# Optimization experiments

Hardware: AMD Instinct MI355X
Metric: run time of the kernel (lower is better)

Reference implementation:

```python
import jax, jax.numpy as jnp
import numpy as np

N_NODES = 50000

def _gcn_layer(x, src, dst, W, b, n_nodes):
    # Linear transform first (PyG GCNConv): h = x @ W
    h = x @ W  # [N, out]
    # Add self-loops
    loop = jnp.arange(n_nodes, dtype=src.dtype)
    src2 = jnp.concatenate([src, loop])
    dst2 = jnp.concatenate([dst, loop])
    # Symmetric normalization deg^-1/2 (deg counts incoming edges incl. self-loop)
    deg = jax.ops.segment_sum(jnp.ones_like(dst2, dtype=h.dtype), dst2, num_segments=n_nodes)
    dinv = jnp.where(deg > 0, jax.lax.rsqrt(deg), 0.0)
    norm = dinv[src2] * dinv[dst2]  # [E+N]
    # Gather-scale-scatter aggregation
    msg = h[src2] * norm[:, None]  # [E+N, out]
    out = jax.ops.segment_sum(msg, dst2, num_segments=n_nodes)
    return out + b

def setup_inputs() -> dict:
    key = jax.random.key(0)
    k1, k2, k3, k4 = jax.random.split(key, 4)
    E = 800000
    x = jax.random.normal(k1, (N_NODES, 128), dtype=jnp.float32)
    edge_index = jax.random.randint(k2, (2, E), 0, N_NODES, dtype=jnp.int64)
    W1 = jax.random.normal(k3, (128, 512), dtype=jnp.float32) * (1.0 / np.sqrt(128))
    b1 = jnp.zeros((512,), dtype=jnp.float32)
    W2 = jax.random.normal(k4, (512, 250), dtype=jnp.float32) * (1.0 / np.sqrt(512))
    b2 = jnp.zeros((250,), dtype=jnp.float32)
    return {"x": x, "edge_index": edge_index, "W1": W1, "b1": b1, "W2": W2, "b2": b2}

def reference(x, edge_index, W1, b1, W2, b2):
    src, dst = edge_index[0], edge_index[1]
    h = _gcn_layer(x, src, dst, W1, b1, N_NODES)
    h = jax.nn.relu(h)
    h = _gcn_layer(h, src, dst, W2, b2, N_NODES)
    return jax.nn.relu(h)
```

## Files before the change

### kernel.cpp

```cpp
#include <hip/hip_runtime.h>

#define N_NODES 50000

typedef __attribute__((ext_vector_type(8))) short bf16x8;
typedef __attribute__((ext_vector_type(4))) float f32x4;

__device__ __forceinline__ ushort f2bf(float f) {
    union { float f; unsigned u; } v; v.f = f;
    unsigned r = v.u + 0x7fff + ((v.u >> 16) & 1);
    return (ushort)(r >> 16);
}
__device__ __forceinline__ float bf2f(ushort u) {
    union { unsigned u; float f; } v; v.u = ((unsigned)u) << 16;
    return v.f;
}
__device__ __forceinline__ float bf2f_lo(unsigned u) {
    union { unsigned u; float f; } v; v.u = u << 16;
    return v.f;
}
__device__ __forceinline__ float bf2f_hi(unsigned u) {
    union { unsigned u; float f; } v; v.u = u & 0xffff0000u;
    return v.f;
}

__global__ void k_detect(const void* ei, int* flag) {
    __shared__ int bad;
    if (threadIdx.x == 0) bad = 0;
    __syncthreads();
    long long v = ((const long long*)ei)[threadIdx.x];
    if (v < 0 || v >= N_NODES) atomicOr(&bad, 1);
    __syncthreads();
    if (threadIdx.x == 0) *flag = bad ? 0 : 1;
}

__device__ __forceinline__ int eload(const void* ei, int idx, int is64) {
    return is64 ? (int)((const long long*)ei)[idx] : ((const int*)ei)[idx];
}

__global__ void k_hist(const void* ei, const int* flag, int* deg, int e) {
    int i = blockIdx.x * blockDim.x + threadIdx.x;
    if (i >= e) return;
    int is64 = *flag;
    int d = eload(ei, e + i, is64);
    atomicAdd(&deg[d], 1);
}

__global__ __launch_bounds__(512)
void k_scanA(const int* __restrict__ deg, int* __restrict__ rp1,
             int* __restrict__ bsum, int n) {
    __shared__ int wsum[8];
    const int i = blockIdx.x * 512 + threadIdx.x;
    const int lane = threadIdx.x & 63, wid = threadIdx.x >> 6;
    int x = (i < n) ? deg[i] : 0;
    #pragma unroll
    for (int off = 1; off < 64; off <<= 1) {
        int y = __shfl_up(x, off, 64);
        if (lane >= off) x += y;
    }
    if (lane == 63) wsum[wid] = x;
    __syncthreads();
    if (wid == 0 && lane < 8) {
        int s = wsum[lane];
        #pragma unroll
        for (int off = 1; off < 8; off <<= 1) {
            int y = __shfl_up(s, off, 64);
            if (lane >= off) s += y;
        }
        wsum[lane] = s;
    }
    __syncthreads();
    int incl = x + (wid > 0 ? wsum[wid - 1] : 0);
    if (i < n) rp1[i] = incl;
    if (threadIdx.x == 0) bsum[blockIdx.x] = wsum[7];
}

__global__ void k_scanB(int* bsum, int nb) {
    __shared__ int ws2[2];
    const int lane = threadIdx.x & 63, wid = threadIdx.x >> 6;
    int x = (threadIdx.x < nb) ? bsum[threadIdx.x] : 0;
    #pragma unroll
    for (int off = 1; off < 64; off <<= 1) {
        int y = __shfl_up(x, off, 64);
        if (lane >= off) x += y;
    }
    if (lane == 63) ws2[wid] = x;
    __syncthreads();
    int incl = x + (wid > 0 ? ws2[0] : 0);
    if (threadIdx.x < nb) bsum[threadIdx.x] = incl;
}

__global__ __launch_bounds__(512)
void k_scanC(const int* __restrict__ deg, int* __restrict__ rowptr,
             const int* __restrict__ bsum, int* __restrict__ cur,
             float* __restrict__ dinv, int n) {
    const int i = blockIdx.x * 512 + threadIdx.x;
    if (i >= n) return;
    const int off = (blockIdx.x > 0) ? bsum[blockIdx.x - 1] : 0;
    const int d = deg[i];
    const int incl = rowptr[i + 1] + off;
    rowptr[i + 1] = incl;
    cur[i] = incl - d;
    dinv[i] = rsqrtf((float)(d + 1));
    if (i == 0) rowptr[0] = 0;
}

__global__ void k_fill(const void* ei, const int* flag, int* cur, int* adj, int e) {
    int i = blockIdx.x * blockDim.x + threadIdx.x;
    if (i >= e) return;
    int is64 = *flag;
    int s = eload(ei, i, is64);
    int d = eload(ei, e + i, is64);
    int pos = atomicAdd(&cur[d], 1);
    adj[pos] = s;
}

__global__ void k_splitT(const float* __restrict__ W, ushort* __restrict__ ohi,
                         ushort* __restrict__ olo, int R , int C ,
                         int Nout ) {
    int idx = blockIdx.x * blockDim.x + threadIdx.x;
    if (idx >= Nout * R) return;
    int n = idx / R;
    int k = idx - n * R;
    float v = (n < C) ? W[(size_t)k * C + n] : 0.0f;
    ushort hi = f2bf(v);
    ohi[idx] = hi;
    olo[idx] = f2bf(v - bf2f(hi));
}

__global__ __launch_bounds__(256)
void k_pull128v(const int* __restrict__ rowptr, const int* __restrict__ adj,
                const float* __restrict__ dinv, const float* __restrict__ x,
                ushort* __restrict__ ohi, int n) {
    const int i = blockIdx.x * 4 + (threadIdx.x >> 6);
    if (i >= n) return;
    const int lane = threadIdx.x & 63;
    const float2* x2 = (const float2*)x;
    const float di = dinv[i];
    float2 v = x2[(size_t)i * 64 + lane];
    float a0 = di * v.x, a1 = di * v.y;
    int j = rowptr[i];
    const int end = rowptr[i + 1];
    for (; j + 8 <= end; j += 8) {
        int s0 = adj[j],     s1 = adj[j + 1], s2 = adj[j + 2], s3 = adj[j + 3];
        int s4 = adj[j + 4], s5 = adj[j + 5], s6 = adj[j + 6], s7 = adj[j + 7];
        float w0 = dinv[s0], w1 = dinv[s1], w2 = dinv[s2], w3 = dinv[s3];
        float w4 = dinv[s4], w5 = dinv[s5], w6 = dinv[s6], w7 = dinv[s7];
        float2 p0 = x2[(size_t)s0 * 64 + lane];
        float2 p1 = x2[(size_t)s1 * 64 + lane];
        float2 p2 = x2[(size_t)s2 * 64 + lane];
        float2 p3 = x2[(size_t)s3 * 64 + lane];
        float2 p4 = x2[(size_t)s4 * 64 + lane];
        float2 p5 = x2[(size_t)s5 * 64 + lane];
        float2 p6 = x2[(size_t)s6 * 64 + lane];
        float2 p7 = x2[(size_t)s7 * 64 + lane];
        a0 += w0 * p0.x + w1 * p1.x + w2 * p2.x + w3 * p3.x;
        a1 += w0 * p0.y + w1 * p1.y + w2 * p2.y + w3 * p3.y;
        a0 += w4 * p4.x + w5 * p5.x + w6 * p6.x + w7 * p7.x;
        a1 += w4 * p4.y + w5 * p5.y + w6 * p6.y + w7 * p7.y;
    }
    for (; j + 4 <= end; j += 4) {
        int s0 = adj[j], s1 = adj[j + 1], s2 = adj[j + 2], s3 = adj[j + 3];
        float w0 = dinv[s0], w1 = dinv[s1], w2 = dinv[s2], w3 = dinv[s3];
        float2 p0 = x2[(size_t)s0 * 64 + lane];
        float2 p1 = x2[(size_t)s1 * 64 + lane];
        float2 p2 = x2[(size_t)s2 * 64 + lane];
        float2 p3 = x2[(size_t)s3 * 64 + lane];
        a0 += w0 * p0.x + w1 * p1.x + w2 * p2.x + w3 * p3.x;
        a1 += w0 * p0.y + w1 * p1.y + w2 * p2.y + w3 * p3.y;
    }
    for (; j < end; ++j) {
        int s = adj[j];
        float w = dinv[s];
        float2 p = x2[(size_t)s * 64 + lane];
        a0 += w * p.x;
        a1 += w * p.y;
    }
    a0 *= di; a1 *= di;
    ((unsigned*)ohi)[(size_t)i * 64 + lane] =
        (unsigned)f2bf(a0) | ((unsigned)f2bf(a1) << 16);
}

__global__ __launch_bounds__(256)
void k_pull250v(const int* __restrict__ rowptr, const int* __restrict__ adj,
                const float* __restrict__ dinv, const ushort* __restrict__ t,
                const float* __restrict__ bias, float* __restrict__ out, int n) {
    const int i = blockIdx.x * 4 + (threadIdx.x >> 6);
    if (i >= n) return;
    const int lane = threadIdx.x & 63;
    const uint2* t2 = (const uint2*)t;
    uint2 u = t2[(size_t)i * 64 + lane];
    float a0 = bf2f_lo(u.x), a1 = bf2f_hi(u.x);
    float a2 = bf2f_lo(u.y), a3 = bf2f_hi(u.y);
    int j = rowptr[i];
    const int end = rowptr[i + 1];
    for (; j + 8 <= end; j += 8) {
        int s0 = adj[j],     s1 = adj[j + 1], s2 = adj[j + 2], s3 = adj[j + 3];
        int s4 = adj[j + 4], s5 = adj[j + 5], s6 = adj[j + 6], s7 = adj[j + 7];
        uint2 u0 = t2[(size_t)s0 * 64 + lane];
        uint2 u1 = t2[(size_t)s1 * 64 + lane];
        uint2 u2 = t2[(size_t)s2 * 64 + lane];
        uint2 u3 = t2[(size_t)s3 * 64 + lane];
        uint2 u4 = t2[(size_t)s4 * 64 + lane];
        uint2 u5 = t2[(size_t)s5 * 64 + lane];
        uint2 u6 = t2[(size_t)s6 * 64 + lane];
        uint2 u7 = t2[(size_t)s7 * 64 + lane];
        a0 += bf2f_lo(u0.x) + bf2f_lo(u1.x) + bf2f_lo(u2.x) + bf2f_lo(u3.x);
        a1 += bf2f_hi(u0.x) + bf2f_hi(u1.x) + bf2f_hi(u2.x) + bf2f_hi(u3.x);
        a2 += bf2f_lo(u0.y) + bf2f_lo(u1.y) + bf2f_lo(u2.y) + bf2f_lo(u3.y);
        a3 += bf2f_hi(u0.y) + bf2f_hi(u1.y) + bf2f_hi(u2.y) + bf2f_hi(u3.y);
        a0 += bf2f_lo(u4.x) + bf2f_lo(u5.x) + bf2f_lo(u6.x) + bf2f_lo(u7.x);
        a1 += bf2f_hi(u4.x) + bf2f_hi(u5.x) + bf2f_hi(u6.x) + bf2f_hi(u7.x);
        a2 += bf2f_lo(u4.y) + bf2f_lo(u5.y) + bf2f_lo(u6.y) + bf2f_lo(u7.y);
        a3 += bf2f_hi(u4.y) + bf2f_hi(u5.y) + bf2f_hi(u6.y) + bf2f_hi(u7.y);
    }
    for (; j + 4 <= end; j += 4) {
        int s0 = adj[j], s1 = adj[j + 1], s2 = adj[j + 2], s3 = adj[j + 3];
        uint2 u0 = t2[(size_t)s0 * 64 + lane];
        uint2 u1 = t2[(size_t)s1 * 64 + lane];
        uint2 u2 = t2[(size_t)s2 * 64 + lane];
        uint2 u3 = t2[(size_t)s3 * 64 + lane];
        a0 += bf2f_lo(u0.x) + bf2f_lo(u1.x) + bf2f_lo(u2.x) + bf2f_lo(u3.x);
        a1 += bf2f_hi(u0.x) + bf2f_hi(u1.x) + bf2f_hi(u2.x) + bf2f_hi(u3.x);
        a2 += bf2f_lo(u0.y) + bf2f_lo(u1.y) + bf2f_lo(u2.y) + bf2f_lo(u3.y);
        a3 += bf2f_hi(u0.y) + bf2f_hi(u1.y) + bf2f_hi(u2.y) + bf2f_hi(u3.y);
    }
    for (; j < end; ++j) {
        uint2 us = t2[(size_t)adj[j] * 64 + lane];
        a0 += bf2f_lo(us.x); a1 += bf2f_hi(us.x);
        a2 += bf2f_lo(us.y); a3 += bf2f_hi(us.y);
    }
    const float d = dinv[i];
    const int c0 = lane * 4;
    if (lane < 62) {
        float2 b0 = *(const float2*)&bias[c0];
        float2 b1 = *(const float2*)&bias[c0 + 2];
        float2 o0, o1;
        o0.x = fmaxf(d * a0 + b0.x, 0.0f);
        o0.y = fmaxf(d * a1 + b0.y, 0.0f);
        o1.x = fmaxf(d * a2 + b1.x, 0.0f);
        o1.y = fmaxf(d * a3 + b1.y, 0.0f);
        *(float2*)&out[(size_t)i * 250 + c0] = o0;
        *(float2*)&out[(size_t)i * 250 + c0 + 2] = o1;
    } else if (lane == 62) {
        float2 b0 = *(const float2*)&bias[248];
        float2 o0;
        o0.x = fmaxf(d * a0 + b0.x, 0.0f);
        o0.y = fmaxf(d * a1 + b0.y, 0.0f);
        *(float2*)&out[(size_t)i * 250 + 248] = o0;
    }
}

__device__ __forceinline__ void gl16(const ushort* g, ushort* l) {
    __builtin_amdgcn_global_load_lds((const __attribute__((address_space(1))) void*)g,
                                     (__attribute__((address_space(3))) void*)l,
                                     16, 0, 0);
}

#define SMEM_HALF 12384

__global__ __launch_bounds__(256, 3)
void k_mfma(const ushort* __restrict__ A, const ushort* __restrict__ Bhi,
            const ushort* __restrict__ Blo, const float* __restrict__ bias,
            const float* __restrict__ rscale, ushort* __restrict__ outp,
            int M, int K, int ldc, int mode, int CX, int PY) {
    __shared__ __align__(16) ushort smem[2 * SMEM_HALF];

    int id = blockIdx.x;
    const int gsz = CX * 8;
    const int nfull = (PY >> 3) * gsz;
    int bx, by;
    if (id < nfull) {
        int gg = id / gsz;
        int r  = id - gg * gsz;
        bx = r >> 3;
        by = gg * 8 + (r & 7);
    } else {
        int rem  = id - nfull;
        int pbase = (PY >> 3) << 3;
        int prem  = PY - pbase;
        by = pbase + rem % prem;
        bx = rem / prem;
    }
    const int brow = by * 128;
    const int bcol = bx * 128;

    const int tid  = threadIdx.x;
    const int lane = tid & 63;
    const int w    = tid >> 6;
    const int g    = lane >> 4;
    const int lr   = lane & 15;
    const int wm   = w >> 1, wn = w & 1;

    const ushort* srcs[3] = {A, Bhi, Blo};

    auto STAGE = [&](ushort* buf, int k0) {
        #pragma unroll
        for (int a = 0; a < 3; ++a) {
            const int rbase = (a == 0) ? brow : bcol;
            #pragma unroll
            for (int t2 = 0; t2 < 2; ++t2) {
                const int b  = w * 2 + t2;
                const int c  = b >> 1;
                const int r0 = (b & 1) * 64;
                gl16(srcs[a] + (size_t)(rbase + r0 + lane) * K + k0 + c * 8,
                     buf + a * 4128 + c * 1032 + r0 * 8);
            }
        }
    };

    f32x4 acc[4][4] = {};

    auto COMPUTE = [&](const ushort* rb) {
        bf16x8 af[4], bhf[4], blf[4];
        #pragma unroll
        for (int i = 0; i < 4; ++i) {
            const int ao = g * 1032 + (wm * 64 + i * 16 + lr) * 8;
            af[i] = *(const bf16x8*)(rb + ao);
            const int bo = g * 1032 + (wn * 64 + i * 16 + lr) * 8;
            bhf[i] = *(const bf16x8*)(rb + 4128 + bo);
            blf[i] = *(const bf16x8*)(rb + 2 * 4128 + bo);
        }
        #pragma unroll
        for (int mt = 0; mt < 4; ++mt)
            #pragma unroll
            for (int nt = 0; nt < 4; ++nt) {
                acc[mt][nt] = __builtin_amdgcn_mfma_f32_16x16x32_bf16(bhf[nt], af[mt], acc[mt][nt], 0, 0, 0);
                acc[mt][nt] = __builtin_amdgcn_mfma_f32_16x16x32_bf16(blf[nt], af[mt], acc[mt][nt], 0, 0, 0);
            }
    };

    STAGE(smem, 0);
    int cur = 0;
    for (int k0 = 32; k0 < K; k0 += 32) {
        STAGE(smem + (cur ^ 1) * SMEM_HALF, k0);
        asm volatile("s_waitcnt vmcnt(6)" ::: "memory");
        __builtin_amdgcn_sched_barrier(0);
        __builtin_amdgcn_s_barrier();
        COMPUTE(smem + cur * SMEM_HALF);
        __builtin_amdgcn_sched_barrier(0);
        __builtin_amdgcn_s_barrier();
        cur ^= 1;
    }
    asm volatile("s_waitcnt vmcnt(0)" ::: "memory");
    __builtin_amdgcn_sched_barrier(0);
    __builtin_amdgcn_s_barrier();
    COMPUTE(smem + cur * SMEM_HALF);

    #pragma unroll
    for (int mt = 0; mt < 4; ++mt) {
        const int gr = brow + wm * 64 + mt * 16 + lr;
        if (gr >= M) continue;
        const float rs = (mode == 0) ? rscale[gr] : 0.0f;
        #pragma unroll
        for (int nt = 0; nt < 4; ++nt) {
            const int gc0 = bcol + wn * 64 + nt * 16 + g * 4;
            float v0, v1, v2, v3;
            if (mode == 0) {
                v0 = acc[mt][nt][0] * rs; v1 = acc[mt][nt][1] * rs;
                v2 = acc[mt][nt][2] * rs; v3 = acc[mt][nt][3] * rs;
            } else {
                const float4 bv = *(const float4*)&bias[gc0];
                v0 = fmaxf(acc[mt][nt][0] + bv.x, 0.0f);
                v1 = fmaxf(acc[mt][nt][1] + bv.y, 0.0f);
                v2 = fmaxf(acc[mt][nt][2] + bv.z, 0.0f);
                v3 = fmaxf(acc[mt][nt][3] + bv.w, 0.0f);
            }
            uint2 pk;
            pk.x = (unsigned)f2bf(v0) | ((unsigned)f2bf(v1) << 16);
            pk.y = (unsigned)f2bf(v2) | ((unsigned)f2bf(v3) << 16);
            *(uint2*)(outp + (size_t)gr * ldc + gc0) = pk;
        }
    }
}

extern "C" void kernel_launch(void* const* d_in, const int* in_sizes, int n_in,
                              void* d_out, int out_size, void* d_ws, size_t ws_size,
                              hipStream_t stream) {
    const float* x  = (const float*)d_in[0];
    const void*  ei = d_in[1];
    const float* W1 = (const float*)d_in[2];
    const float* b1 = (const float*)d_in[3];
    const float* W2 = (const float*)d_in[4];
    const float* b2 = (const float*)d_in[5];
    float* out = (float*)d_out;

    const int N = N_NODES;
    const int E = in_sizes[1] / 2;
    const int MPAD = 50048;
    const int NSCB = (N + 511) / 512;

    char* base = (char*)d_ws;
    int*   flag   = (int*)base;
    int*   deg    = (int*)(base + 256);
    int*   rowptr = deg + 51200;
    int*   cur    = rowptr + 51200;
    float* dinv   = (float*)(cur + 51200);
    int*   bsum   = (int*)(dinv + 51200);
    int*   adj    = bsum + 128;
    char*  p      = (char*)(adj + ((E + 63) & ~63));
    ushort* A1hi  = (ushort*)p;  p += (size_t)MPAD * 128 * 2;
    ushort* A1xx  = (ushort*)p;  p += (size_t)MPAD * 128 * 2;
    ushort* tbuf  = A1hi;
    ushort* h1hi  = (ushort*)p;  p += (size_t)MPAD * 512 * 2;
    ushort* Bt1hi = (ushort*)p;  p += 512 * 128 * 2;
    ushort* Bt1lo = (ushort*)p;  p += 512 * 128 * 2;
    ushort* Bt2hi = (ushort*)p;  p += 256 * 512 * 2;
    ushort* Bt2lo = (ushort*)p;  p += 256 * 512 * 2;
    (void)A1xx;

    k_detect<<<1, 1024, 0, stream>>>(ei, flag);
    hipMemsetAsync(deg, 0, (size_t)N * sizeof(int), stream);
    k_hist<<<(E + 255) / 256, 256, 0, stream>>>(ei, flag, deg, E);
    k_scanA<<<NSCB, 512, 0, stream>>>(deg, rowptr + 1, bsum, N);
    k_scanB<<<1, 128, 0, stream>>>(bsum, NSCB);
    k_scanC<<<NSCB, 512, 0, stream>>>(deg, rowptr, bsum, cur, dinv, N);
    k_fill<<<(E + 255) / 256, 256, 0, stream>>>(ei, flag, cur, adj, E);

    k_splitT<<<(512 * 128 + 255) / 256, 256, 0, stream>>>(W1, Bt1hi, Bt1lo, 128, 512, 512);
    k_splitT<<<(256 * 512 + 255) / 256, 256, 0, stream>>>(W2, Bt2hi, Bt2lo, 512, 250, 256);

    k_pull128v<<<(N + 3) / 4, 256, 0, stream>>>(rowptr, adj, dinv, x, A1hi, N);

    k_mfma<<<4 * 391, 256, 0, stream>>>(A1hi, Bt1hi, Bt1lo, b1, nullptr, h1hi,
                                        N, 128, 512, 1, 4, 391);

    k_mfma<<<2 * 391, 256, 0, stream>>>(h1hi, Bt2hi, Bt2lo, nullptr, dinv, tbuf,
                                        N, 512, 256, 0, 2, 391);

    k_pull250v<<<(N + 3) / 4, 256, 0, stream>>>(rowptr, adj, dinv, tbuf, b2, out, N);
}
```

Before: 317.5 us.

## Widen MFMA GEMM tile to 128x256 with each wave covering full M

The bf16 split-precision GEMM kernel's block tile grows from 128x128 to 128x256. Each of the four waves now computes all 128 rows against its own 64-column slice, so A fragments are reused across more B columns. The LDS layout drops the padded 1032 stride, the waitcnt is adjusted for the extra loads, and launch bounds fall to 2 blocks per CU. The aim is fewer A reloads and more MFMA work per LDS read. The cost is doubled accumulator registers, lower occupancy, possible LDS bank conflicts from removing the padding, and fewer blocks (391 for the second GEMM), which may underfill the GPU.

```diff
diff --git a/kernel.cpp b/kernel.cpp
--- a/kernel.cpp
+++ b/kernel.cpp
@@ -256,9 +256,11 @@
                                      16, 0, 0);
 }
 
-#define SMEM_HALF 12384
-
-__global__ __launch_bounds__(256, 3)
+#define OFF_BH 4096
+#define OFF_BL 12288
+#define SMEM_HALF 20480
+
+__global__ __launch_bounds__(256, 2)
 void k_mfma(const ushort* __restrict__ A, const ushort* __restrict__ Bhi,
             const ushort* __restrict__ Blo, const float* __restrict__ bias,
             const float* __restrict__ rscale, ushort* __restrict__ outp,
@@ -282,50 +284,49 @@
         bx = rem / prem;
     }
     const int brow = by * 128;
-    const int bcol = bx * 128;
+    const int bcol = bx * 256;
 
     const int tid  = threadIdx.x;
     const int lane = tid & 63;
     const int w    = tid >> 6;
     const int g    = lane >> 4;
     const int lr   = lane & 15;
-    const int wm   = w >> 1, wn = w & 1;
-
-    const ushort* srcs[3] = {A, Bhi, Blo};
 
     auto STAGE = [&](ushort* buf, int k0) {
-        #pragma unroll
-        for (int a = 0; a < 3; ++a) {
-            const int rbase = (a == 0) ? brow : bcol;
-            #pragma unroll
-            for (int t2 = 0; t2 < 2; ++t2) {
-                const int b  = w * 2 + t2;
-                const int c  = b >> 1;
-                const int r0 = (b & 1) * 64;
-                gl16(srcs[a] + (size_t)(rbase + r0 + lane) * K + k0 + c * 8,
-                     buf + a * 4128 + c * 1032 + r0 * 8);
-            }
+        const int kofs = k0 + w * 8;
+        #pragma unroll
+        for (int t2 = 0; t2 < 2; ++t2)
+            gl16(A + (size_t)(brow + t2 * 64 + lane) * K + kofs,
+                 buf + w * 1024 + t2 * 512);
+        #pragma unroll
+        for (int t4 = 0; t4 < 4; ++t4)
+            gl16(Bhi + (size_t)(bcol + t4 * 64 + lane) * K + kofs,
+                 buf + OFF_BH + w * 2048 + t4 * 512);
+        #pragma unroll
+        for (int t4 = 0; t4 < 4; ++t4)
+            gl16(Blo + (size_t)(bcol + t4 * 64 + lane) * K + kofs,
+                 buf + OFF_BL + w * 2048 + t4 * 512);
+    };
+
+    f32x4 acc[8][4] = {};
+
+    auto COMPUTE = [&](const ushort* rb) {
+        bf16x8 af[8], bh[4], bl[4];
+        #pragma unroll
+        for (int nt = 0; nt < 4; ++nt) {
+            const int bo = g * 2048 + (w * 64 + nt * 16 + lr) * 8;
+            bh[nt] = *(const bf16x8*)(rb + OFF_BH + bo);
+            bl[nt] = *(const bf16x8*)(rb + OFF_BL + bo);
         }
-    };
-
-    f32x4 acc[4][4] = {};
-
-    auto COMPUTE = [&](const ushort* rb) {
-        bf16x8 af[4], bhf[4], blf[4];
-        #pragma unroll
-        for (int i = 0; i < 4; ++i) {
-            const int ao = g * 1032 + (wm * 64 + i * 16 + lr) * 8;
-            af[i] = *(const bf16x8*)(rb + ao);
-            const int bo = g * 1032 + (wn * 64 + i * 16 + lr) * 8;
-            bhf[i] = *(const bf16x8*)(rb + 4128 + bo);
-            blf[i] = *(const bf16x8*)(rb + 2 * 4128 + bo);
-        }
-        #pragma unroll
-        for (int mt = 0; mt < 4; ++mt)
+        #pragma unroll
+        for (int mt = 0; mt < 8; ++mt)
+            af[mt] = *(const bf16x8*)(rb + g * 1024 + (mt * 16 + lr) * 8);
+        #pragma unroll
+        for (int mt = 0; mt < 8; ++mt)
             #pragma unroll
             for (int nt = 0; nt < 4; ++nt) {
-                acc[mt][nt] = __builtin_amdgcn_mfma_f32_16x16x32_bf16(bhf[nt], af[mt], acc[mt][nt], 0, 0, 0);
-                acc[mt][nt] = __builtin_amdgcn_mfma_f32_16x16x32_bf16(blf[nt], af[mt], acc[mt][nt], 0, 0, 0);
+                acc[mt][nt] = __builtin_amdgcn_mfma_f32_16x16x32_bf16(bh[nt], af[mt], acc[mt][nt], 0, 0, 0);
+                acc[mt][nt] = __builtin_amdgcn_mfma_f32_16x16x32_bf16(bl[nt], af[mt], acc[mt][nt], 0, 0, 0);
             }
     };
 
@@ -333,7 +334,7 @@
     int cur = 0;
     for (int k0 = 32; k0 < K; k0 += 32) {
         STAGE(smem + (cur ^ 1) * SMEM_HALF, k0);
-        asm volatile("s_waitcnt vmcnt(6)" ::: "memory");
+        asm volatile("s_waitcnt vmcnt(10)" ::: "memory");
         __builtin_amdgcn_sched_barrier(0);
         __builtin_amdgcn_s_barrier();
         COMPUTE(smem + cur * SMEM_HALF);
@@ -347,13 +348,13 @@
     COMPUTE(smem + cur * SMEM_HALF);
 
     #pragma unroll
-    for (int mt = 0; mt < 4; ++mt) {
-        const int gr = brow + wm * 64 + mt * 16 + lr;
+    for (int mt = 0; mt < 8; ++mt) {
+        const int gr = brow + mt * 16 + lr;
         if (gr >= M) continue;
         const float rs = (mode == 0) ? rscale[gr] : 0.0f;
         #pragma unroll
         for (int nt = 0; nt < 4; ++nt) {
-            const int gc0 = bcol + wn * 64 + nt * 16 + g * 4;
+            const int gc0 = bcol + w * 64 + nt * 16 + g * 4;
             float v0, v1, v2, v3;
             if (mode == 0) {
                 v0 = acc[mt][nt][0] * rs; v1 = acc[mt][nt][1] * rs;
@@ -421,11 +422,11 @@
 
     k_pull128v<<<(N + 3) / 4, 256, 0, stream>>>(rowptr, adj, dinv, x, A1hi, N);
 
-    k_mfma<<<4 * 391, 256, 0, stream>>>(A1hi, Bt1hi, Bt1lo, b1, nullptr, h1hi,
-                                        N, 128, 512, 1, 4, 391);
-
-    k_mfma<<<2 * 391, 256, 0, stream>>>(h1hi, Bt2hi, Bt2lo, nullptr, dinv, tbuf,
-                                        N, 512, 256, 0, 2, 391);
+    k_mfma<<<2 * 391, 256, 0, stream>>>(A1hi, Bt1hi, Bt1lo, b1, nullptr, h1hi,
+                                        N, 128, 512, 1, 2, 391);
+
+    k_mfma<<<1 * 391, 256, 0, stream>>>(h1hi, Bt2hi, Bt2lo, nullptr, dinv, tbuf,
+                                        N, 512, 256, 0, 1, 391);
 
     k_pull250v<<<(N + 3) / 4, 256, 0, stream>>>(rowptr, adj, dinv, tbuf, b2, out, N);
 }
```

Measured after the change: 326.9 us. 1.03x slower.
